# Optimization experiments

Measured on AMD Instinct MI355X. Metric: run time of the kernel, lower is better.

Reference implementation:

```python
import jax, jax.numpy as jnp
import numpy as np

N_NODES = 50000
N_EDGES = 800000
IN_C, HID_C, OUT_C = 128, 128, 64


def setup_inputs() -> dict:
    key = jax.random.key(0)
    ks = jax.random.split(key, 8)
    x = jax.random.normal(ks[0], (N_NODES, IN_C), dtype=jnp.float32)
    edge_index = jax.random.randint(ks[1], (2, N_EDGES), 0, N_NODES, dtype=jnp.int64)
    def glorot(k, shape):
        lim = np.sqrt(6.0 / (shape[0] + shape[1])).astype(np.float32)
        return jax.random.uniform(k, shape, jnp.float32, -lim, lim)
    return {
        "x": x,
        "edge_index": edge_index,
        "W1l": glorot(ks[2], (IN_C, HID_C)),
        "b1": jnp.zeros((HID_C,), jnp.float32),
        "W1r": glorot(ks[3], (IN_C, HID_C)),
        "W2l": glorot(ks[4], (HID_C, OUT_C)),
        "b2": jnp.zeros((OUT_C,), jnp.float32),
        "W2r": glorot(ks[5], (HID_C, OUT_C)),
    }


def _sage_conv(h, src, dst, Wl, bl, Wr):
    # mean aggregation over incoming edges (source -> target)
    n = h.shape[0]
    msg_sum = jax.ops.segment_sum(h[src], dst, num_segments=n)          # [N, d]
    deg = jax.ops.segment_sum(jnp.ones((src.shape[0],), h.dtype), dst, num_segments=n)
    agg = msg_sum / jnp.maximum(deg, 1.0)[:, None]                      # zero-degree -> 0
    # lin_l(agg) + lin_r(h); lin_l carries the bias (PyG SAGEConv default)
    return agg @ Wl + bl + h @ Wr


def reference(x, edge_index, W1l, b1, W1r, W2l, b2, W2r):
    src, dst = edge_index[0], edge_index[1]
    h = jax.nn.relu(_sage_conv(x, src, dst, W1l, b1, W1r))
    # eval-mode forward: dropout is identity
    out = _sage_conv(h, src, dst, W2l, b2, W2r)
    return out
```

## Files before the change

### kernel.cpp

```cpp
#include <hip/hip_runtime.h>

#define N_NODES 50000
#define N_EDGES 800000
#define IN_C    128
#define HID_C   128
#define OUT_C   64
#define NBUCK   196
#define BCAP    6144
#define QCAP    1536
#define EPB     2048
#define EBLKS   ((N_EDGES + EPB - 1) / EPB)
#define PACK_BLKS 192
#define MM1_BLKS  ((N_NODES + 63) / 64)
#define L2F_BLKS  (NBUCK * 4)
#define HS_STRIDE 136

typedef unsigned short ushort_t;
typedef unsigned int   uint_t;
typedef unsigned char  uchar_t;
typedef __attribute__((ext_vector_type(8))) short bf16x8;
typedef __attribute__((ext_vector_type(4))) float f32x4;
typedef __attribute__((ext_vector_type(2))) float f32x2;

__device__ inline ushort_t f2bf(float f) {
    uint_t u = __float_as_uint(f);
    uint_t r = (u + 0x7fffu + ((u >> 16) & 1u)) >> 16;
    return (ushort_t)r;
}
__device__ inline float bflo(uint_t v) { return __uint_as_float(v << 16); }
__device__ inline float bfhi(uint_t v) { return __uint_as_float(v & 0xffff0000u); }
__device__ inline uchar_t f2fp8(float v) {
    return (uchar_t)(__builtin_amdgcn_cvt_pk_fp8_f32(v, v, 0, false) & 0xff);
}
__device__ inline void acc_fp8x4(float* a, uint_t d) {
    const f32x2 lo = __builtin_amdgcn_cvt_pk_f32_fp8((int)d, false);
    const f32x2 hi = __builtin_amdgcn_cvt_pk_f32_fp8((int)d, true);
    a[0] += lo.x; a[1] += lo.y; a[2] += hi.x; a[3] += hi.y;
}

__device__ inline void pack_one(const float* W, ushort_t* Wp, int K, int N, int idx) {
    const int j  = idx & 7;
    const int L  = (idx >> 3) & 63;
    const int t  = idx >> 9;
    const int KT = K / 32;
    const int kt = t % KT;
    const int ct = t / KT;
    const int k  = kt * 32 + (L >> 4) * 8 + j;
    const int n  = ct * 16 + (L & 15);
    Wp[idx] = f2bf(W[k * N + n]);
}

__global__ __launch_bounds__(256) void k0_kernel(
    const float* __restrict__ W1l, const float* __restrict__ W1r,
    const float* __restrict__ W2l, const float* __restrict__ W2r,
    ushort_t* __restrict__ wpack, int* __restrict__ gcur)
{
    const int b = blockIdx.x;
    if (b < PACK_BLKS) {
        const int tid = b * 256 + threadIdx.x;
        if (tid < 16384)      pack_one(W1l, wpack,          IN_C,  HID_C, tid);
        else if (tid < 32768) pack_one(W1r, wpack + 16384,  IN_C,  HID_C, tid - 16384);
        else if (tid < 40960) pack_one(W2l, wpack + 32768,  HID_C, OUT_C, tid - 32768);
        else if (tid < 49152) pack_one(W2r, wpack + 40960,  HID_C, OUT_C, tid - 40960);
    } else {
        if (threadIdx.x < NBUCK) gcur[threadIdx.x] = 0;
    }
}

__device__ inline void mm1_body(int bid, const float* __restrict__ x,
                                const ushort_t* __restrict__ wpack,
                                uchar_t* __restrict__ p1f, ushort_t* __restrict__ t1b)
{
    const int wave = threadIdx.x >> 6;
    const int lane = threadIdx.x & 63;
    const int quad = lane >> 4;
    const int m    = lane & 15;
    const int row0 = bid * 64 + wave * 16;
    const int arow = min(row0 + m, N_NODES - 1);

    const bf16x8* Bl = (const bf16x8*)(wpack);
    const bf16x8* Br = (const bf16x8*)(wpack + 16384);

    f32x4 accl[8], accr[8];
#pragma unroll
    for (int ct = 0; ct < 8; ++ct) { accl[ct] = (f32x4)(0.0f); accr[ct] = (f32x4)(0.0f); }

#pragma unroll
    for (int kt = 0; kt < 4; ++kt) {
        const float* xp = x + (size_t)arow * IN_C + kt * 32 + quad * 8;
        const float4 a0 = *(const float4*)(xp);
        const float4 a1 = *(const float4*)(xp + 4);
        bf16x8 af;
        af[0] = (short)f2bf(a0.x); af[1] = (short)f2bf(a0.y);
        af[2] = (short)f2bf(a0.z); af[3] = (short)f2bf(a0.w);
        af[4] = (short)f2bf(a1.x); af[5] = (short)f2bf(a1.y);
        af[6] = (short)f2bf(a1.z); af[7] = (short)f2bf(a1.w);
#pragma unroll
        for (int ct = 0; ct < 8; ++ct) {
            const bf16x8 bl = Bl[(ct * 4 + kt) * 64 + lane];
            const bf16x8 br = Br[(ct * 4 + kt) * 64 + lane];
            accl[ct] = __builtin_amdgcn_mfma_f32_16x16x32_bf16(af, bl, accl[ct], 0, 0, 0);
            accr[ct] = __builtin_amdgcn_mfma_f32_16x16x32_bf16(af, br, accr[ct], 0, 0, 0);
        }
    }

#pragma unroll
    for (int r = 0; r < 4; ++r) {
        const int orow = row0 + quad * 4 + r;
        if (orow < N_NODES) {
#pragma unroll
            for (int ct = 0; ct < 8; ++ct) {
                const int col = ct * 16 + m;
                p1f[(size_t)orow * HID_C + col] = f2fp8(accl[ct][r]);
                t1b[(size_t)orow * HID_C + col] = f2bf(accr[ct][r]);
            }
        }
    }
}

__global__ __launch_bounds__(256) void k1_kernel(
    const float* __restrict__ x, const ushort_t* __restrict__ wpack,
    uchar_t* __restrict__ p1f, ushort_t* __restrict__ t1b,
    const int* __restrict__ src, const int* __restrict__ dst,
    int* gcur, int* __restrict__ ebuf)
{
    __shared__ int lh[256], gbase[256], lcur[256];
    const int b = blockIdx.x;
    if (b < MM1_BLKS) {
        mm1_body(b, x, wpack, p1f, t1b);
        return;
    }
    const int blk = b - MM1_BLKS;
    const int t = threadIdx.x;
    lh[t] = 0;
    __syncthreads();
    const int e0 = blk * EPB + t * 8;
    int v8[8], b8[8];
    if (e0 < N_EDGES) {
        const int4 sa = *(const int4*)&src[e0];
        const int4 sb = *(const int4*)&src[e0 + 4];
        const int4 da = *(const int4*)&dst[e0];
        const int4 db = *(const int4*)&dst[e0 + 4];
        const int s8a[8] = {sa.x, sa.y, sa.z, sa.w, sb.x, sb.y, sb.z, sb.w};
        const int d8a[8] = {da.x, da.y, da.z, da.w, db.x, db.y, db.z, db.w};
#pragma unroll
        for (int j = 0; j < 8; ++j) {
            b8[j] = d8a[j] >> 8;
            v8[j] = (s8a[j] << 8) | (d8a[j] & 255);
            atomicAdd(&lh[b8[j]], 1);
        }
    } else {
#pragma unroll
        for (int j = 0; j < 8; ++j) b8[j] = -1;
    }
    __syncthreads();
    if (t < NBUCK) {
        const int run = lh[t];
        gbase[t] = (run > 0) ? atomicAdd(&gcur[t], run) : 0;
        lcur[t] = 0;
    }
    __syncthreads();
#pragma unroll
    for (int j = 0; j < 8; ++j) {
        const int bk = b8[j];
        if (bk >= 0) {
            const int p = atomicAdd(&lcur[bk], 1);
            ebuf[bk * BCAP + gbase[bk] + p] = v8[j];
        }
    }
}

__global__ __launch_bounds__(256, 4) void l2f_kernel(
    const int* __restrict__ ebuf, const int* __restrict__ gcur,
    int* __restrict__ cnt, int* __restrict__ row_ptr, int* __restrict__ csr_g,
    const uchar_t* __restrict__ p1f, const ushort_t* __restrict__ t1b,
    const float* __restrict__ b1,
    const ushort_t* __restrict__ wpack,
    uchar_t* __restrict__ p2f, ushort_t* __restrict__ t2b)
{
    __shared__ ushort_t hs[64 * HS_STRIDE];
    __shared__ int csr_lds[QCAP];
    __shared__ int lh[64], lstart[64], lcur2[64];
    __shared__ int pool;

    const int blk    = blockIdx.x;
    const int bucket = blk >> 2;
    const int q      = blk & 3;
    const int tid    = threadIdx.x;

    if (tid == 0) pool = 0;
    if (tid < 64) lh[tid] = 0;
    __syncthreads();

    const int eb0 = bucket * BCAP;
    const int nb  = gcur[bucket];
    for (int i = tid; i < nb; i += 256) {
        const int d = ebuf[eb0 + i] & 255;
        if ((d >> 6) == q) atomicAdd(&lh[d & 63], 1);
    }
    __syncthreads();
    int scanv = 0;
    if (tid < 64) scanv = lh[tid];
    if (tid < 64) lcur2[tid] = scanv;
    __syncthreads();
#pragma unroll
    for (int off = 1; off < 64; off <<= 1) {
        int add = 0;
        if (tid < 64 && tid >= off) add = lcur2[tid - off];
        __syncthreads();
        if (tid < 64) lcur2[tid] += add;
        __syncthreads();
    }
    if (tid < 64) {
        const int ex = lcur2[tid] - scanv;
        lstart[tid] = ex;
        const int node = blk * 64 + tid;
        if (node < N_NODES) { cnt[node] = scanv; row_ptr[node] = blk * QCAP + ex; }
    }
    __syncthreads();
    if (tid < 64) lcur2[tid] = lstart[tid];
    __syncthreads();
    for (int i = tid; i < nb; i += 256) {
        const int v = ebuf[eb0 + i];
        const int d = v & 255;
        if ((d >> 6) == q) {
            const int p = atomicAdd(&lcur2[d & 63], 1);
            if (p < QCAP) csr_lds[p] = v >> 8;
        }
    }
    __syncthreads();
    {
        const int total = lcur2[63] > QCAP ? QCAP : lcur2[63];
        for (int i = tid; i < total; i += 256) csr_g[blk * QCAP + i] = csr_lds[i];
    }
    __syncthreads();

    const int c16 = tid & 7;
    const int gb  = (tid & 63) & 56;
    const uint4* p1v = (const uint4*)p1f;

    while (true) {
        int nl = 0;
        if (c16 == 0) nl = atomicAdd(&pool, 1);
        nl = __shfl(nl, gb, 64);
        if (nl >= 64) break;
        const int node = blk * 64 + nl;
        uint4 oL = make_uint4(0u, 0u, 0u, 0u);
        uint4 oH = make_uint4(0u, 0u, 0u, 0u);
        if (node < N_NODES) {
            const int start = lstart[nl];
            const int degi  = lh[nl];
            float a[16];
#pragma unroll
            for (int z = 0; z < 16; ++z) a[z] = 0.0f;
            int e = 0;
            for (; e + 3 < degi; e += 4) {
                const int s0 = csr_lds[start + e];
                const int s1 = csr_lds[start + e + 1];
                const int s2 = csr_lds[start + e + 2];
                const int s3 = csr_lds[start + e + 3];
                const uint4 v0 = p1v[(size_t)s0 * 8 + c16];
                const uint4 v1 = p1v[(size_t)s1 * 8 + c16];
                const uint4 v2 = p1v[(size_t)s2 * 8 + c16];
                const uint4 v3 = p1v[(size_t)s3 * 8 + c16];
#pragma unroll
                for (int qq = 0; qq < 4; ++qq) {
                    const uint4 v = (qq == 0) ? v0 : (qq == 1) ? v1 : (qq == 2) ? v2 : v3;
                    acc_fp8x4(a + 0,  v.x);
                    acc_fp8x4(a + 4,  v.y);
                    acc_fp8x4(a + 8,  v.z);
                    acc_fp8x4(a + 12, v.w);
                }
            }
            for (; e < degi; ++e) {
                const uint4 v = p1v[(size_t)csr_lds[start + e] * 8 + c16];
                acc_fp8x4(a + 0,  v.x);
                acc_fp8x4(a + 4,  v.y);
                acc_fp8x4(a + 8,  v.z);
                acc_fp8x4(a + 12, v.w);
            }
            const float inv = 1.0f / fmaxf((float)degi, 1.0f);
            const size_t i = (size_t)node * HID_C + c16 * 16;
            const uint4 tvL = *(const uint4*)(t1b + i);
            const uint4 tvH = *(const uint4*)(t1b + i + 8);
            float r[16];
#pragma unroll
            for (int z = 0; z < 4; ++z) {
                const float4 bv = *(const float4*)(b1 + c16 * 16 + z * 4);
                const uint_t t01 = (z < 2) ? ((z == 0) ? tvL.x : tvL.y)
                                           : ((z == 2) ? tvH.x : tvH.y);
                (void)t01;
                r[z*4+0] = bv.x; r[z*4+1] = bv.y; r[z*4+2] = bv.z; r[z*4+3] = bv.w;
            }
            const uint_t tw[8] = {tvL.x, tvL.y, tvL.z, tvL.w, tvH.x, tvH.y, tvH.z, tvH.w};
#pragma unroll
            for (int z = 0; z < 8; ++z) {
                r[z*2+0] = fmaxf(fmaf(a[z*2+0], inv, r[z*2+0] + bflo(tw[z])), 0.0f);
                r[z*2+1] = fmaxf(fmaf(a[z*2+1], inv, r[z*2+1] + bfhi(tw[z])), 0.0f);
            }
            oL.x = (uint_t)f2bf(r[0])  | ((uint_t)f2bf(r[1])  << 16);
            oL.y = (uint_t)f2bf(r[2])  | ((uint_t)f2bf(r[3])  << 16);
            oL.z = (uint_t)f2bf(r[4])  | ((uint_t)f2bf(r[5])  << 16);
            oL.w = (uint_t)f2bf(r[6])  | ((uint_t)f2bf(r[7])  << 16);
            oH.x = (uint_t)f2bf(r[8])  | ((uint_t)f2bf(r[9])  << 16);
            oH.y = (uint_t)f2bf(r[10]) | ((uint_t)f2bf(r[11]) << 16);
            oH.z = (uint_t)f2bf(r[12]) | ((uint_t)f2bf(r[13]) << 16);
            oH.w = (uint_t)f2bf(r[14]) | ((uint_t)f2bf(r[15]) << 16);
        }
        *(uint4*)&hs[nl * HS_STRIDE + c16 * 16] = oL;
        *(uint4*)&hs[nl * HS_STRIDE + c16 * 16 + 8] = oH;
    }
    __syncthreads();

    const int wv   = tid >> 6;
    const int lane = tid & 63;
    const int quad = lane >> 4;
    const int m    = lane & 15;
    const int row0 = blk * 64 + wv * 16;

    const bf16x8* Bl = (const bf16x8*)(wpack + 32768);
    const bf16x8* Br = (const bf16x8*)(wpack + 40960);

    f32x4 accl[4], accr[4];
#pragma unroll
    for (int ct = 0; ct < 4; ++ct) { accl[ct] = (f32x4)(0.0f); accr[ct] = (f32x4)(0.0f); }

#pragma unroll
    for (int kt = 0; kt < 4; ++kt) {
        const bf16x8 af = *(const bf16x8*)&hs[(wv * 16 + m) * HS_STRIDE + kt * 32 + quad * 8];
#pragma unroll
        for (int ct = 0; ct < 4; ++ct) {
            const bf16x8 bl = Bl[(ct * 4 + kt) * 64 + lane];
            const bf16x8 br = Br[(ct * 4 + kt) * 64 + lane];
            accl[ct] = __builtin_amdgcn_mfma_f32_16x16x32_bf16(af, bl, accl[ct], 0, 0, 0);
            accr[ct] = __builtin_amdgcn_mfma_f32_16x16x32_bf16(af, br, accr[ct], 0, 0, 0);
        }
    }

#pragma unroll
    for (int r = 0; r < 4; ++r) {
        const int orow = row0 + quad * 4 + r;
        if (orow < N_NODES) {
#pragma unroll
            for (int ct = 0; ct < 4; ++ct) {
                const int col = ct * 16 + m;
                p2f[(size_t)orow * OUT_C + col] = f2fp8(accl[ct][r]);
                t2b[(size_t)orow * OUT_C + col] = f2bf(accr[ct][r]);
            }
        }
    }
}

__global__ __launch_bounds__(256) void agg2_kernel(
    const uchar_t* __restrict__ p2f, const ushort_t* __restrict__ t2b,
    const float* __restrict__ b2, const int* __restrict__ row_ptr,
    const int* __restrict__ cnt, const int* __restrict__ csr,
    float* __restrict__ out)
{
    const int c16 = threadIdx.x & 3;
    const int grp = threadIdx.x >> 2;
    const uint4* p2v = (const uint4*)p2f;

    const int node = blockIdx.x * 64 + grp;
    if (node >= N_NODES) return;
    const int start = row_ptr[node];
    const int degi  = cnt[node];
    float a[16];
#pragma unroll
    for (int z = 0; z < 16; ++z) a[z] = 0.0f;
    int e = 0;
    for (; e + 3 < degi; e += 4) {
        const int s0 = csr[start + e];
        const int s1 = csr[start + e + 1];
        const int s2 = csr[start + e + 2];
        const int s3 = csr[start + e + 3];
        const uint4 v0 = p2v[(size_t)s0 * 4 + c16];
        const uint4 v1 = p2v[(size_t)s1 * 4 + c16];
        const uint4 v2 = p2v[(size_t)s2 * 4 + c16];
        const uint4 v3 = p2v[(size_t)s3 * 4 + c16];
#pragma unroll
        for (int q = 0; q < 4; ++q) {
            const uint4 v = (q == 0) ? v0 : (q == 1) ? v1 : (q == 2) ? v2 : v3;
            acc_fp8x4(a + 0,  v.x);
            acc_fp8x4(a + 4,  v.y);
            acc_fp8x4(a + 8,  v.z);
            acc_fp8x4(a + 12, v.w);
        }
    }
    for (; e < degi; ++e) {
        const uint4 v = p2v[(size_t)csr[start + e] * 4 + c16];
        acc_fp8x4(a + 0,  v.x);
        acc_fp8x4(a + 4,  v.y);
        acc_fp8x4(a + 8,  v.z);
        acc_fp8x4(a + 12, v.w);
    }

    const float inv = 1.0f / fmaxf((float)degi, 1.0f);
    const size_t i = (size_t)node * OUT_C + c16 * 16;
    const uint4 tvL = *(const uint4*)(t2b + i);
    const uint4 tvH = *(const uint4*)(t2b + i + 8);
    const uint_t tw[8] = {tvL.x, tvL.y, tvL.z, tvL.w, tvH.x, tvH.y, tvH.z, tvH.w};
#pragma unroll
    for (int z = 0; z < 4; ++z) {
        const float4 bv = *(const float4*)(b2 + c16 * 16 + z * 4);
        float4 o;
        o.x = fmaf(a[z*4+0], inv, bv.x + bflo(tw[z*2+0]));
        o.y = fmaf(a[z*4+1], inv, bv.y + bfhi(tw[z*2+0]));
        o.z = fmaf(a[z*4+2], inv, bv.z + bflo(tw[z*2+1]));
        o.w = fmaf(a[z*4+3], inv, bv.w + bfhi(tw[z*2+1]));
        *(float4*)(out + i + z * 4) = o;
    }
}

extern "C" void kernel_launch(void* const* d_in, const int* in_sizes, int n_in,
                              void* d_out, int out_size, void* d_ws, size_t ws_size,
                              hipStream_t stream)
{
    const float* x   = (const float*)d_in[0];
    const int*   ei  = (const int*)d_in[1];
    const float* W1l = (const float*)d_in[2];
    const float* b1  = (const float*)d_in[3];
    const float* W1r = (const float*)d_in[4];
    const float* W2l = (const float*)d_in[5];
    const float* b2  = (const float*)d_in[6];
    const float* W2r = (const float*)d_in[7];
    float* out = (float*)d_out;

    const int* src = ei;
    const int* dst = ei + N_EDGES;

    const size_t NH = (size_t)N_NODES * HID_C;
    const size_t NO = (size_t)N_NODES * OUT_C;
    const size_t EB = (size_t)NBUCK * BCAP;
    const size_t CB = (size_t)L2F_BLKS * QCAP;

    char* ws = (char*)d_ws;
    ushort_t* t1b   = (ushort_t*)ws;                   ws += NH * sizeof(ushort_t);
    ushort_t* t2b   = (ushort_t*)ws;                   ws += NO * sizeof(ushort_t);
    ushort_t* wpack = (ushort_t*)ws;                   ws += 49152 * sizeof(ushort_t);
    int* ebuf    = (int*)ws;                           ws += EB * sizeof(int);
    int* csr     = (int*)ws;                           ws += CB * sizeof(int);
    int* cnt     = (int*)ws;                           ws += N_NODES * sizeof(int);
    int* row_ptr = (int*)ws;                           ws += N_NODES * sizeof(int);
    int* gcur    = (int*)ws;                           ws += NBUCK * sizeof(int);
    ws += (16 - ((size_t)(ws - (char*)d_ws) & 15)) & 15;
    uchar_t* p1f = (uchar_t*)ws;                       ws += NH * sizeof(uchar_t);
    uchar_t* p2f = (uchar_t*)ws;                       ws += NO * sizeof(uchar_t);

    const size_t need = (size_t)(ws - (char*)d_ws);
    if (ws_size < need) return;

    k0_kernel<<<PACK_BLKS + 1, 256, 0, stream>>>(W1l, W1r, W2l, W2r, wpack, gcur);
    k1_kernel<<<MM1_BLKS + EBLKS, 256, 0, stream>>>(
        x, wpack, p1f, t1b, src, dst, gcur, ebuf);
    l2f_kernel<<<L2F_BLKS, 256, 0, stream>>>(
        ebuf, gcur, cnt, row_ptr, csr, p1f, t1b, b1, wpack, p2f, t2b);
    agg2_kernel<<<MM1_BLKS, 256, 0, stream>>>(
        p2f, t2b, b2, row_ptr, cnt, csr, out);
}
```

Baseline: 160.4 us.

## Bucket edges by 64-node quarter directly so each block reads only its own edges

The edge scatter in k1 now buckets edges into 784 buckets of 64 destination nodes instead of 196 buckets of 256. Each l2f block then reads only its own edge list once into registers and reuses it for both the histogram and the CSR fill, instead of scanning a 4x larger bucket twice and filtering. Per-node t1b/t2b loads are also hoisted ahead of the gather loops so they can overlap with it. The cost is more shared-memory histogram bins and global atomics in k1. A per-bucket capacity cap now silently drops edges if a bucket ever overflows 1536 entries.

```diff
diff --git a/kernel.cpp b/kernel.cpp
--- a/kernel.cpp
+++ b/kernel.cpp
@@ -5,14 +5,14 @@
 #define IN_C    128
 #define HID_C   128
 #define OUT_C   64
-#define NBUCK   196
-#define BCAP    6144
+#define NQ      784
+#define QBCAP   1536
 #define QCAP    1536
 #define EPB     2048
 #define EBLKS   ((N_EDGES + EPB - 1) / EPB)
 #define PACK_BLKS 192
 #define MM1_BLKS  ((N_NODES + 63) / 64)
-#define L2F_BLKS  (NBUCK * 4)
+#define L2F_BLKS  NQ
 #define HS_STRIDE 136
 
 typedef unsigned short ushort_t;
@@ -63,7 +63,7 @@
         else if (tid < 40960) pack_one(W2l, wpack + 32768,  HID_C, OUT_C, tid - 32768);
         else if (tid < 49152) pack_one(W2r, wpack + 40960,  HID_C, OUT_C, tid - 40960);
     } else {
-        if (threadIdx.x < NBUCK) gcur[threadIdx.x] = 0;
+        for (int i = threadIdx.x; i < NQ; i += 256) gcur[i] = 0;
     }
 }
 
@@ -124,7 +124,7 @@
     const int* __restrict__ src, const int* __restrict__ dst,
     int* gcur, int* __restrict__ ebuf)
 {
-    __shared__ int lh[256], gbase[256], lcur[256];
+    __shared__ int lh[NQ], gb2[NQ], lc[NQ];
     const int b = blockIdx.x;
     if (b < MM1_BLKS) {
         mm1_body(b, x, wpack, p1f, t1b);
@@ -132,7 +132,7 @@
     }
     const int blk = b - MM1_BLKS;
     const int t = threadIdx.x;
-    lh[t] = 0;
+    for (int i = t; i < NQ; i += 256) lh[i] = 0;
     __syncthreads();
     const int e0 = blk * EPB + t * 8;
     int v8[8], b8[8];
@@ -145,8 +145,8 @@
         const int d8a[8] = {da.x, da.y, da.z, da.w, db.x, db.y, db.z, db.w};
 #pragma unroll
         for (int j = 0; j < 8; ++j) {
-            b8[j] = d8a[j] >> 8;
-            v8[j] = (s8a[j] << 8) | (d8a[j] & 255);
+            b8[j] = d8a[j] >> 6;
+            v8[j] = (s8a[j] << 6) | (d8a[j] & 63);
             atomicAdd(&lh[b8[j]], 1);
         }
     } else {
@@ -154,18 +154,19 @@
         for (int j = 0; j < 8; ++j) b8[j] = -1;
     }
     __syncthreads();
-    if (t < NBUCK) {
-        const int run = lh[t];
-        gbase[t] = (run > 0) ? atomicAdd(&gcur[t], run) : 0;
-        lcur[t] = 0;
+    for (int i = t; i < NQ; i += 256) {
+        const int run = lh[i];
+        gb2[i] = (run > 0) ? atomicAdd(&gcur[i], run) : 0;
+        lc[i] = 0;
     }
     __syncthreads();
 #pragma unroll
     for (int j = 0; j < 8; ++j) {
         const int bk = b8[j];
         if (bk >= 0) {
-            const int p = atomicAdd(&lcur[bk], 1);
-            ebuf[bk * BCAP + gbase[bk] + p] = v8[j];
+            const int p   = atomicAdd(&lc[bk], 1);
+            const int pos = gb2[bk] + p;
+            if (pos < QBCAP) ebuf[bk * QBCAP + pos] = v8[j];
         }
     }
 }
@@ -183,21 +184,28 @@
     __shared__ int lh[64], lstart[64], lcur2[64];
     __shared__ int pool;
 
-    const int blk    = blockIdx.x;
-    const int bucket = blk >> 2;
-    const int q      = blk & 3;
-    const int tid    = threadIdx.x;
+    const int blk = blockIdx.x;
+    const int tid = threadIdx.x;
 
     if (tid == 0) pool = 0;
     if (tid < 64) lh[tid] = 0;
     __syncthreads();
 
-    const int eb0 = bucket * BCAP;
-    const int nb  = gcur[bucket];
-    for (int i = tid; i < nb; i += 256) {
-        const int d = ebuf[eb0 + i] & 255;
-        if ((d >> 6) == q) atomicAdd(&lh[d & 63], 1);
-    }
+    const int nb   = min(gcur[blk], QBCAP);
+    const int base = blk * QBCAP;
+    int v0 = -1, v1 = -1, v2 = -1, v3 = -1, v4 = -1, v5 = -1;
+    if (tid        < nb) v0 = ebuf[base + tid];
+    if (tid + 256  < nb) v1 = ebuf[base + tid + 256];
+    if (tid + 512  < nb) v2 = ebuf[base + tid + 512];
+    if (tid + 768  < nb) v3 = ebuf[base + tid + 768];
+    if (tid + 1024 < nb) v4 = ebuf[base + tid + 1024];
+    if (tid + 1280 < nb) v5 = ebuf[base + tid + 1280];
+    if (v0 >= 0) atomicAdd(&lh[v0 & 63], 1);
+    if (v1 >= 0) atomicAdd(&lh[v1 & 63], 1);
+    if (v2 >= 0) atomicAdd(&lh[v2 & 63], 1);
+    if (v3 >= 0) atomicAdd(&lh[v3 & 63], 1);
+    if (v4 >= 0) atomicAdd(&lh[v4 & 63], 1);
+    if (v5 >= 0) atomicAdd(&lh[v5 & 63], 1);
     __syncthreads();
     int scanv = 0;
     if (tid < 64) scanv = lh[tid];
@@ -220,14 +228,12 @@
     __syncthreads();
     if (tid < 64) lcur2[tid] = lstart[tid];
     __syncthreads();
-    for (int i = tid; i < nb; i += 256) {
-        const int v = ebuf[eb0 + i];
-        const int d = v & 255;
-        if ((d >> 6) == q) {
-            const int p = atomicAdd(&lcur2[d & 63], 1);
-            if (p < QCAP) csr_lds[p] = v >> 8;
-        }
-    }
+    if (v0 >= 0) { const int p = atomicAdd(&lcur2[v0 & 63], 1); if (p < QCAP) csr_lds[p] = v0 >> 6; }
+    if (v1 >= 0) { const int p = atomicAdd(&lcur2[v1 & 63], 1); if (p < QCAP) csr_lds[p] = v1 >> 6; }
+    if (v2 >= 0) { const int p = atomicAdd(&lcur2[v2 & 63], 1); if (p < QCAP) csr_lds[p] = v2 >> 6; }
+    if (v3 >= 0) { const int p = atomicAdd(&lcur2[v3 & 63], 1); if (p < QCAP) csr_lds[p] = v3 >> 6; }
+    if (v4 >= 0) { const int p = atomicAdd(&lcur2[v4 & 63], 1); if (p < QCAP) csr_lds[p] = v4 >> 6; }
+    if (v5 >= 0) { const int p = atomicAdd(&lcur2[v5 & 63], 1); if (p < QCAP) csr_lds[p] = v5 >> 6; }
     __syncthreads();
     {
         const int total = lcur2[63] > QCAP ? QCAP : lcur2[63];
@@ -250,6 +256,9 @@
         if (node < N_NODES) {
             const int start = lstart[nl];
             const int degi  = lh[nl];
+            const size_t ib = (size_t)node * HID_C + c16 * 16;
+            const uint4 tvL = *(const uint4*)(t1b + ib);
+            const uint4 tvH = *(const uint4*)(t1b + ib + 8);
             float a[16];
 #pragma unroll
             for (int z = 0; z < 16; ++z) a[z] = 0.0f;
@@ -259,13 +268,13 @@
                 const int s1 = csr_lds[start + e + 1];
                 const int s2 = csr_lds[start + e + 2];
                 const int s3 = csr_lds[start + e + 3];
-                const uint4 v0 = p1v[(size_t)s0 * 8 + c16];
-                const uint4 v1 = p1v[(size_t)s1 * 8 + c16];
-                const uint4 v2 = p1v[(size_t)s2 * 8 + c16];
-                const uint4 v3 = p1v[(size_t)s3 * 8 + c16];
+                const uint4 w0 = p1v[(size_t)s0 * 8 + c16];
+                const uint4 w1 = p1v[(size_t)s1 * 8 + c16];
+                const uint4 w2 = p1v[(size_t)s2 * 8 + c16];
+                const uint4 w3 = p1v[(size_t)s3 * 8 + c16];
 #pragma unroll
                 for (int qq = 0; qq < 4; ++qq) {
-                    const uint4 v = (qq == 0) ? v0 : (qq == 1) ? v1 : (qq == 2) ? v2 : v3;
+                    const uint4 v = (qq == 0) ? w0 : (qq == 1) ? w1 : (qq == 2) ? w2 : w3;
                     acc_fp8x4(a + 0,  v.x);
                     acc_fp8x4(a + 4,  v.y);
                     acc_fp8x4(a + 8,  v.z);
@@ -280,16 +289,10 @@
                 acc_fp8x4(a + 12, v.w);
             }
             const float inv = 1.0f / fmaxf((float)degi, 1.0f);
-            const size_t i = (size_t)node * HID_C + c16 * 16;
-            const uint4 tvL = *(const uint4*)(t1b + i);
-            const uint4 tvH = *(const uint4*)(t1b + i + 8);
             float r[16];
 #pragma unroll
             for (int z = 0; z < 4; ++z) {
                 const float4 bv = *(const float4*)(b1 + c16 * 16 + z * 4);
-                const uint_t t01 = (z < 2) ? ((z == 0) ? tvL.x : tvL.y)
-                                           : ((z == 2) ? tvH.x : tvH.y);
-                (void)t01;
                 r[z*4+0] = bv.x; r[z*4+1] = bv.y; r[z*4+2] = bv.z; r[z*4+3] = bv.w;
             }
             const uint_t tw[8] = {tvL.x, tvL.y, tvL.z, tvL.w, tvH.x, tvH.y, tvH.z, tvH.w};
@@ -365,6 +368,9 @@
     if (node >= N_NODES) return;
     const int start = row_ptr[node];
     const int degi  = cnt[node];
+    const size_t i = (size_t)node * OUT_C + c16 * 16;
+    const uint4 tvL = *(const uint4*)(t2b + i);
+    const uint4 tvH = *(const uint4*)(t2b + i + 8);
     float a[16];
 #pragma unroll
     for (int z = 0; z < 16; ++z) a[z] = 0.0f;
@@ -374,13 +380,13 @@
         const int s1 = csr[start + e + 1];
         const int s2 = csr[start + e + 2];
         const int s3 = csr[start + e + 3];
-        const uint4 v0 = p2v[(size_t)s0 * 4 + c16];
-        const uint4 v1 = p2v[(size_t)s1 * 4 + c16];
-        const uint4 v2 = p2v[(size_t)s2 * 4 + c16];
-        const uint4 v3 = p2v[(size_t)s3 * 4 + c16];
+        const uint4 w0 = p2v[(size_t)s0 * 4 + c16];
+        const uint4 w1 = p2v[(size_t)s1 * 4 + c16];
+        const uint4 w2 = p2v[(size_t)s2 * 4 + c16];
+        const uint4 w3 = p2v[(size_t)s3 * 4 + c16];
 #pragma unroll
         for (int q = 0; q < 4; ++q) {
-            const uint4 v = (q == 0) ? v0 : (q == 1) ? v1 : (q == 2) ? v2 : v3;
+            const uint4 v = (q == 0) ? w0 : (q == 1) ? w1 : (q == 2) ? w2 : w3;
             acc_fp8x4(a + 0,  v.x);
             acc_fp8x4(a + 4,  v.y);
             acc_fp8x4(a + 8,  v.z);
@@ -396,9 +402,6 @@
     }
 
     const float inv = 1.0f / fmaxf((float)degi, 1.0f);
-    const size_t i = (size_t)node * OUT_C + c16 * 16;
-    const uint4 tvL = *(const uint4*)(t2b + i);
-    const uint4 tvH = *(const uint4*)(t2b + i + 8);
     const uint_t tw[8] = {tvL.x, tvL.y, tvL.z, tvL.w, tvH.x, tvH.y, tvH.z, tvH.w};
 #pragma unroll
     for (int z = 0; z < 4; ++z) {
@@ -431,8 +434,8 @@
 
     const size_t NH = (size_t)N_NODES * HID_C;
     const size_t NO = (size_t)N_NODES * OUT_C;
-    const size_t EB = (size_t)NBUCK * BCAP;
-    const size_t CB = (size_t)L2F_BLKS * QCAP;
+    const size_t EB = (size_t)NQ * QBCAP;
+    const size_t CB = (size_t)NQ * QCAP;
 
     char* ws = (char*)d_ws;
     ushort_t* t1b   = (ushort_t*)ws;                   ws += NH * sizeof(ushort_t);
@@ -442,7 +445,7 @@
     int* csr     = (int*)ws;                           ws += CB * sizeof(int);
     int* cnt     = (int*)ws;                           ws += N_NODES * sizeof(int);
     int* row_ptr = (int*)ws;                           ws += N_NODES * sizeof(int);
-    int* gcur    = (int*)ws;                           ws += NBUCK * sizeof(int);
+    int* gcur    = (int*)ws;                           ws += NQ * sizeof(int);
     ws += (16 - ((size_t)(ws - (char*)d_ws) & 15)) & 15;
     uchar_t* p1f = (uchar_t*)ws;                       ws += NH * sizeof(uchar_t);
     uchar_t* p2f = (uchar_t*)ws;                       ws += NO * sizeof(uchar_t);
```

After: 155.3 us. -3.2%, faster.
